# Kernel tuning notes

Hardware: AMD Instinct MI355X
Metric: run time of the kernel (lower is better)

The kernel has to match this reference:

```python
import jax, jax.numpy as jnp
import numpy as np

B, N, M, D, NH, HD = 2, 1024, 1024, 1536, 16, 96
RD = HD // 3  # per-axis rotary dim = 32
EPS = 1e-6
SCALE = HD ** -0.5


def _rmsnorm(y, w):
    return y * jax.lax.rsqrt(jnp.mean(y * y, axis=-1, keepdims=True) + EPS) * w


def _rope_tables(T, H, W):
    # inv_freqs identical for t/h/w since all three dims are RD
    inv_f = 1.0 / (10000.0 ** (jnp.arange(0, RD, 2, dtype=jnp.float32)[: RD // 2] / RD))
    gt, gh, gw = jnp.meshgrid(
        jnp.arange(T, dtype=jnp.float32),
        jnp.arange(H, dtype=jnp.float32),
        jnp.arange(W, dtype=jnp.float32),
        indexing='ij')
    ft = gt.reshape(-1, 1) * inv_f[None, :]  # [L, RD//2]
    fh = gh.reshape(-1, 1) * inv_f[None, :]
    fw = gw.reshape(-1, 1) * inv_f[None, :]
    return (jnp.cos(ft), jnp.sin(ft), jnp.cos(fh), jnp.sin(fh), jnp.cos(fw), jnp.sin(fw))


def _apply_rope(xq, cos, sin):
    # xq: [B, L, NH, RD]; cos/sin: [L, RD//2]
    c = jnp.concatenate([cos, cos], axis=-1)[None, :, None, :]
    s = jnp.concatenate([sin, sin], axis=-1)[None, :, None, :]
    x1, x2 = jnp.split(xq, 2, axis=-1)
    rot = jnp.concatenate([-x2, x1], axis=-1)
    return xq * c + rot * s


def setup_inputs() -> dict:
    key = jax.random.key(0)
    ks = jax.random.split(key, 10)
    w = lambda k: jax.random.normal(k, (D, D), dtype=jnp.float32) * 0.02
    return {
        'cond': jax.random.normal(ks[0], (B, N, D), dtype=jnp.float32),
        'x': jax.random.normal(ks[1], (B, M, D), dtype=jnp.float32),
        'cond_q_w': w(ks[2]), 'cond_k_w': w(ks[3]), 'cond_v_w': w(ks[4]),
        'cond_qnorm_w': jnp.ones((D,), jnp.float32),
        'cond_knorm_w': jnp.ones((D,), jnp.float32),
        'cond_proj_w': w(ks[5]),
        'x_q_w': w(ks[6]), 'x_k_w': w(ks[7]), 'x_v_w': w(ks[8]),
        'x_qnorm_w': jnp.ones((D,), jnp.float32),
        'x_knorm_w': jnp.ones((D,), jnp.float32),
        'x_proj_w': w(ks[9]),
        'T': 2, 'H': 32, 'W': 32,
    }


def reference(cond, x, cond_q_w, cond_k_w, cond_v_w, cond_qnorm_w, cond_knorm_w,
              cond_proj_w, x_q_w, x_k_w, x_v_w, x_qnorm_w, x_knorm_w, x_proj_w,
              T, H, W):
    # dual-stream QKV + RMSNorm (qkv_bias=False, eval -> no dropout)
    cq = _rmsnorm(cond @ cond_q_w, cond_qnorm_w).reshape(B, N, NH, HD)
    ck = _rmsnorm(cond @ cond_k_w, cond_knorm_w).reshape(B, N, NH, HD)
    cv = (cond @ cond_v_w).reshape(B, N, NH, HD)
    xq = _rmsnorm(x @ x_q_w, x_qnorm_w).reshape(B, M, NH, HD)
    xk = _rmsnorm(x @ x_k_w, x_knorm_w).reshape(B, M, NH, HD)
    xv = (x @ x_v_w).reshape(B, M, NH, HD)

    q = jnp.concatenate([cq, xq], axis=1)  # [B, N+M, NH, HD]
    k = jnp.concatenate([ck, xk], axis=1)
    v = jnp.concatenate([cv, xv], axis=1)

    # 3D RoPE: split head_dim into t/h/w thirds and rotate each with its own freqs
    cos_t, sin_t, cos_h, sin_h, cos_w, sin_w = _rope_tables(T, H, W)
    qt, qh, qw = jnp.split(q, 3, axis=-1)
    kt, kh, kw = jnp.split(k, 3, axis=-1)
    q = jnp.concatenate([_apply_rope(qt, cos_t, sin_t),
                         _apply_rope(qh, cos_h, sin_h),
                         _apply_rope(qw, cos_w, sin_w)], axis=-1)
    k = jnp.concatenate([_apply_rope(kt, cos_t, sin_t),
                         _apply_rope(kh, cos_h, sin_h),
                         _apply_rope(kw, cos_w, sin_w)], axis=-1)

    # joint non-causal SDPA
    scores = jnp.einsum('blhd,bmhd->bhlm', q, k) * SCALE
    attn = jax.nn.softmax(scores, axis=-1)
    out = jnp.einsum('bhlm,bmhd->blhd', attn, v).reshape(B, N + M, D)

    cond_out = out[:, :N] @ cond_proj_w
    x_out = out[:, N:] @ x_proj_w
    return cond_out, x_out
```

## Files before the change

kernel.cpp:

```cpp
#include <hip/hip_runtime.h>
#include <stdint.h>

#define DEV __device__ __forceinline__

using f32x4  = __attribute__((ext_vector_type(4))) float;
using f32x16 = __attribute__((ext_vector_type(16))) float;
using bf16x8 = __attribute__((ext_vector_type(8))) short;

DEV ushort f2bf(float f){
  uint32_t u = __float_as_uint(f);
  u += 0x7FFFu + ((u >> 16) & 1u);
  return (ushort)(u >> 16);
}
DEV float bf2f(ushort h){ return __uint_as_float(((uint32_t)h) << 16); }

DEV void async16(const void* g, void* l){
  __builtin_amdgcn_global_load_lds(
      (const __attribute__((address_space(1))) void*)g,
      (__attribute__((address_space(3))) void*)l, 16, 0, 0);
}

union FU { uint4 u; bf16x8 v; };
DEV bf16x8 as_bf16x8(uint a, uint b, uint c, uint d){ FU f; f.u = make_uint4(a,b,c,d); return f.v; }

__global__ __launch_bounds__(256) void k_conv_in(const float* __restrict__ src, ushort* __restrict__ dst){
  int i = (blockIdx.x * 256 + threadIdx.x) * 8;
  float4 a = *(const float4*)(src + i);
  float4 b = *(const float4*)(src + i + 4);
  union { ushort s[8]; uint4 q; } o;
  o.s[0]=f2bf(a.x); o.s[1]=f2bf(a.y); o.s[2]=f2bf(a.z); o.s[3]=f2bf(a.w);
  o.s[4]=f2bf(b.x); o.s[5]=f2bf(b.y); o.s[6]=f2bf(b.z); o.s[7]=f2bf(b.w);
  *(uint4*)(dst + i) = o.q;
}

__global__ __launch_bounds__(256) void k_transpose_w(
    const float* w0, const float* w1, const float* w2, const float* w3,
    const float* w4, const float* w5, const float* w6, const float* w7,
    ushort* __restrict__ dst){
  __shared__ float tile[32][33];
  int z = blockIdx.z;
  const float* src = (z==0)?w0:(z==1)?w1:(z==2)?w2:(z==3)?w3:(z==4)?w4:(z==5)?w5:(z==6)?w6:w7;
  int n0 = blockIdx.x * 32;
  int k0 = blockIdx.y * 32;
  int tx = threadIdx.x;
  int ty = threadIdx.y;
  for (int j = 0; j < 4; ++j)
    tile[ty + j*8][tx] = src[(size_t)(k0 + ty + j*8) * 1536 + n0 + tx];
  __syncthreads();
  ushort* d = dst + (size_t)z * 1536 * 1536;
  for (int j = 0; j < 4; ++j){
    int n = n0 + ty + j*8;
    int k = k0 + tx;
    d[(size_t)n * 1536 + k] = f2bf(tile[tx][ty + j*8]);
  }
}

__global__ __launch_bounds__(512, 2) void k_gemm_qkv(const ushort* __restrict__ inb,
                                                     const ushort* __restrict__ Wt,
                                                     ushort* __restrict__ Y){
  __shared__ ushort As[2][16384];
  __shared__ ushort Bs[2][18432];
  int f = blockIdx.x;
  int nid = (f & 7) * 32 + (f >> 3);
  int z = nid >> 7; int r = nid & 127;
  int my = (r >> 2) & 7, nx = (r >> 5) * 4 + (r & 3);
  const ushort* A = inb + (size_t)z * 2048 * 1536 + (size_t)(my * 256) * 1536;
  const ushort* B = Wt  + (size_t)z * 4608 * 1536 + (size_t)(nx * 288) * 1536;
  ushort* Yt = Y + (size_t)z * 2048 * 4608 + (size_t)(my * 256) * 4608 + nx * 288;
  int tid = threadIdx.x;
  int w = tid >> 6, lane = tid & 63;
  int g = lane >> 4, fr = lane & 15;
  int wm = (w >> 1) * 64, wn = (w & 1) * 144;

  f32x4 acc[4][9] = {};

  auto stageA = [&](int b, int kt){
#pragma unroll
    for (int s = 0; s < 4; ++s){
      int c = s * 512 + tid;
      int row = c >> 3, ch = c & 7;
      async16(A + (size_t)row * 1536 + kt + ((ch ^ (row & 7)) * 8), &As[b][(s*512 + w*64) * 8]);
    }
  };
  auto stageB = [&](int b, int kt){
#pragma unroll
    for (int s = 0; s < 4; ++s){
      int c = s * 512 + tid;
      int row = c >> 3, ch = c & 7;
      async16(B + (size_t)row * 1536 + kt + ((ch ^ (row & 7)) * 8), &Bs[b][(s*512 + w*64) * 8]);
    }
    if (tid < 256){
      int c = 2048 + tid;
      int row = c >> 3, ch = c & 7;
      async16(B + (size_t)row * 1536 + kt + ((ch ^ (row & 7)) * 8), &Bs[b][(2048 + w*64) * 8]);
    }
  };

  stageA(0, 0); stageB(0, 0);
  asm volatile("s_waitcnt vmcnt(0)" ::: "memory");
  __builtin_amdgcn_s_barrier();
  asm volatile("" ::: "memory");

  for (int t = 0; t < 24; ++t){
    int cur = t & 1; int kt1 = (t + 1) * 64;
#pragma unroll
    for (int ks = 0; ks < 2; ++ks){
      bf16x8 af[4], bf[9];
#pragma unroll
      for (int j = 0; j < 4; ++j){
        int row = wm + j*16 + fr;
        af[j] = *(const bf16x8*)&As[cur][(row*8 + ((ks*4 + g) ^ (row & 7))) * 8];
      }
#pragma unroll
      for (int ni = 0; ni < 9; ++ni){
        int row = wn + ni*16 + fr;
        bf[ni] = *(const bf16x8*)&Bs[cur][(row*8 + ((ks*4 + g) ^ (row & 7))) * 8];
      }
      if (t < 23){
        if (ks == 0) stageA(cur ^ 1, kt1);
        else stageB(cur ^ 1, kt1);
      }
      asm volatile("" ::: "memory");
      __builtin_amdgcn_s_barrier();
      asm volatile("" ::: "memory");
      __builtin_amdgcn_s_setprio(1);
#pragma unroll
      for (int ni = 0; ni < 9; ++ni){
#pragma unroll
        for (int j = 0; j < 4; ++j)
          acc[j][ni] = __builtin_amdgcn_mfma_f32_16x16x32_bf16(af[j], bf[ni], acc[j][ni], 0, 0, 0);
      }
      __builtin_amdgcn_s_setprio(0);
      if (ks == 1) asm volatile("s_waitcnt vmcnt(0)" ::: "memory");
      asm volatile("" ::: "memory");
      __builtin_amdgcn_s_barrier();
      asm volatile("" ::: "memory");
    }
  }

#pragma unroll
  for (int mi = 0; mi < 4; ++mi)
#pragma unroll
    for (int ni = 0; ni < 9; ++ni)
#pragma unroll
      for (int rr = 0; rr < 4; ++rr)
        Yt[(size_t)(wm + mi*16 + g*4 + rr) * 4608 + wn + ni*16 + fr] = f2bf(acc[mi][ni][rr]);
}

template<bool OUT_BF16>
DEV void gemm_tile(const ushort* __restrict__ A, const ushort* __restrict__ Bt, void* __restrict__ Cp,
                   int K, int lda, int ldb, int ldc, int m0, int n0){
  __shared__ ushort As[8192];
  __shared__ ushort Bs[8192];
  int tid = threadIdx.x;
  int w = tid >> 6, lane = tid & 63;
  int g = lane >> 4, fr = lane & 15;
  int wm = (w >> 1) * 64, wn = (w & 1) * 64;
  f32x4 acc[4][4] = {};
  for (int kt = 0; kt < K; kt += 64){
    __syncthreads();
#pragma unroll
    for (int i = 0; i < 4; ++i){
      int ci = i * 256 + tid;
      int row = ci >> 3, ch = ci & 7;
      int src8 = (ch ^ (row & 7)) * 8;
      async16(A  + (size_t)(m0 + row) * lda + kt + src8, As + (i*256 + w*64) * 8);
      async16(Bt + (size_t)(n0 + row) * ldb + kt + src8, Bs + (i*256 + w*64) * 8);
    }
    __syncthreads();
#pragma unroll
    for (int ks = 0; ks < 2; ++ks){
      bf16x8 af[4], bf[4];
      int cidx = ((ks*4 + g) ^ (fr & 7)) * 8;
#pragma unroll
      for (int mi = 0; mi < 4; ++mi) af[mi] = *(const bf16x8*)(As + (wm + mi*16 + fr) * 64 + cidx);
#pragma unroll
      for (int ni = 0; ni < 4; ++ni) bf[ni] = *(const bf16x8*)(Bs + (wn + ni*16 + fr) * 64 + cidx);
#pragma unroll
      for (int mi = 0; mi < 4; ++mi)
#pragma unroll
        for (int ni = 0; ni < 4; ++ni)
          acc[mi][ni] = __builtin_amdgcn_mfma_f32_16x16x32_bf16(af[mi], bf[ni], acc[mi][ni], 0, 0, 0);
    }
  }
  int cr = (lane >> 4) * 4, cc2 = lane & 15;
#pragma unroll
  for (int mi = 0; mi < 4; ++mi)
#pragma unroll
    for (int ni = 0; ni < 4; ++ni)
#pragma unroll
      for (int r = 0; r < 4; ++r){
        size_t idx = (size_t)(m0 + wm + mi*16 + cr + r) * ldc + (n0 + wn + ni*16 + cc2);
        if (OUT_BF16) ((ushort*)Cp)[idx] = f2bf(acc[mi][ni][r]);
        else          ((float*)Cp)[idx]  = acc[mi][ni][r];
      }
}

__global__ __launch_bounds__(256) void k_gemm_proj(const ushort* __restrict__ AO, const ushort* __restrict__ Wtp,
                                                   float* __restrict__ out){
  int f = blockIdx.x;
  int nid = (f & 7) * 48 + (f >> 3);
  int z = nid / 96; int rr = nid - z * 96;
  int by = rr / 12; int bx = rr - by * 12;
  int s = z >> 1, bb = z & 1;
  gemm_tile<false>(AO + (size_t)(bb*2048 + s*1024) * 1536, Wtp + (size_t)s * 1536 * 1536,
                   (void*)(out + (size_t)(s*2048 + bb*1024) * 1536), 1536, 1536, 1536, 1536,
                   by * 128, bx * 128);
}

__global__ __launch_bounds__(256) void k_norm_rope(
    const ushort* __restrict__ Y,
    const float* __restrict__ qn_c, const float* __restrict__ kn_c,
    const float* __restrict__ qn_x, const float* __restrict__ kn_x,
    ushort* __restrict__ Qb, ushort* __restrict__ Kb, ushort* __restrict__ Vb){
  int r = blockIdx.x;
  int z = blockIdx.y;
  const ushort* y = Y + ((size_t)z * 2048 + r) * 4608;
  const float* qw = z ? qn_x : qn_c;
  const float* kw = z ? kn_x : kn_c;
  int b = r >> 10;
  int l = (z << 10) + (r & 1023);
  int tid = threadIdx.x;
  __shared__ float cs[48], sn[48];
  if (tid < 48){
    int axis = tid >> 4, fj = tid & 15;
    int pos = (axis == 0) ? (l >> 10) : ((axis == 1) ? ((l >> 5) & 31) : (l & 31));
    float inv = __expf(-(float)fj * 0.5756462732485114f);
    float a = (float)pos * inv;
    sn[tid] = sinf(a); cs[tid] = cosf(a);
  }
  float yq1[3], yq2[3], yk1[3], yk2[3];
  float ssq = 0.f, ssk = 0.f;
#pragma unroll
  for (int i = 0; i < 3; ++i){
    int p = tid + i*256;
    int head = p / 48, rem = p % 48;
    int c1 = head*96 + (rem >> 4)*32 + (rem & 15);
    float a1 = bf2f(y[c1]),        a2 = bf2f(y[c1 + 16]);
    float b1 = bf2f(y[1536 + c1]), b2 = bf2f(y[1536 + c1 + 16]);
    yq1[i]=a1; yq2[i]=a2; yk1[i]=b1; yk2[i]=b2;
    ssq += a1*a1 + a2*a2;
    ssk += b1*b1 + b2*b2;
  }
#pragma unroll
  for (int mm = 1; mm < 64; mm <<= 1){
    ssq += __shfl_xor(ssq, mm);
    ssk += __shfl_xor(ssk, mm);
  }
  __shared__ float red[8];
  int w = tid >> 6;
  if ((tid & 63) == 0){ red[w] = ssq; red[4 + w] = ssk; }
  __syncthreads();
  float scq = rsqrtf((red[0]+red[1]+red[2]+red[3]) * (1.f/1536.f) + 1e-6f);
  float sck = rsqrtf((red[4]+red[5]+red[6]+red[7]) * (1.f/1536.f) + 1e-6f);
  float scqS = scq * 0.1020620726159658f;
#pragma unroll
  for (int i = 0; i < 3; ++i){
    int p = tid + i*256;
    int head = p / 48, rem = p % 48;
    int axis = rem >> 4, fj = rem & 15;
    int c1 = head*96 + axis*32 + fj;
    float c = cs[rem], s = sn[rem];
    size_t rowb = ((size_t)(b*16 + head) * 2048 + l) * 96;
    float a1 = yq1[i] * scqS * qw[c1], a2 = yq2[i] * scqS * qw[c1 + 16];
    Qb[rowb + axis*32 + fj]      = f2bf(a1*c - a2*s);
    Qb[rowb + axis*32 + fj + 16] = f2bf(a2*c + a1*s);
    float b1 = yk1[i] * sck * kw[c1], b2 = yk2[i] * sck * kw[c1 + 16];
    int d1 = axis*32 + fj;
    Kb[rowb + d1]      = f2bf(b1*c - b2*s);
    Kb[rowb + d1 + 16] = f2bf(b2*c + b1*s);
  }
#pragma unroll
  for (int i = 0; i < 6; ++i){
    int cidx = tid + i*256;
    int head = cidx / 96, hd = cidx - head*96;
    Vb[((size_t)(b*16 + head) * 2048 + l) * 96 + hd] = y[3072 + cidx];
  }
}

__global__ __launch_bounds__(256) void k_transpose_v(const ushort* __restrict__ V, ushort* __restrict__ Vt){
  __shared__ ushort t[32][33];
  int bh = blockIdx.z;
  const ushort* src = V + (size_t)bh * 2048 * 96;
  ushort* dst = Vt + (size_t)bh * 96 * 2048;
  int c0 = blockIdx.x * 32;
  int r0 = blockIdx.y * 32;
  int tx = threadIdx.x, ty = threadIdx.y;
  for (int j = 0; j < 4; ++j)
    t[ty + j*8][tx] = src[(size_t)(r0 + ty + j*8) * 96 + c0 + tx];
  __syncthreads();
  for (int j = 0; j < 4; ++j){
    int d = c0 + ty + j*8;
    int l = r0 + tx;
    dst[(size_t)d * 2048 + l] = t[tx][ty + j*8];
  }
}

__global__ __launch_bounds__(256, 2) void k_attn(const ushort* __restrict__ Qb, const ushort* __restrict__ Kb,
                                                 const ushort* __restrict__ Vt, ushort* __restrict__ AO){
  __shared__ ushort Ks[2][6400];
  __shared__ ushort Vs[2][6528];
  int id = blockIdx.x;
  int nid = (id & 7) * 64 + (id >> 3);
  int qt = nid & 15, bh = nid >> 4;
  int b = bh >> 4, head = bh & 15;
  const ushort* Qh = Qb + (size_t)bh * 2048 * 96;
  const ushort* Kh = Kb + (size_t)bh * 2048 * 96;
  const ushort* Vh = Vt + (size_t)bh * 96 * 2048;
  int tid = threadIdx.x;
  int w = tid >> 6, lane = tid & 63;
  int h = lane >> 5, c = lane & 31;
  int q0 = qt * 128 + w * 32;

  bf16x8 qf[6];
#pragma unroll
  for (int kb = 0; kb < 6; ++kb)
    qf[kb] = *(const bf16x8*)(Qh + (size_t)(q0 + c) * 96 + kb*16 + h*8);

  int gko[3], lko[3], gvo[3], lvo[3];
#pragma unroll
  for (int i = 0; i < 3; ++i){
    int fc = i*256 + tid;
    int krow = (fc * 683) >> 13;
    int kc8  = (fc - krow*12) * 8;
    gko[i] = krow*96 + kc8;
    lko[i] = krow*100 + kc8;
    int vrow = fc >> 3;
    int vc8  = (fc & 7) * 8;
    gvo[i] = vrow*2048 + vc8;
    lvo[i] = vrow*68 + (vc8 ^ ((vrow & 7) << 3));
  }
  uint4 kst[3], vst[3];

  auto LOADG = [&](int tt){
#pragma unroll
    for (int i = 0; i < 3; ++i){
      kst[i] = *(const uint4*)(Kh + (size_t)tt*6144 + gko[i]);
      vst[i] = *(const uint4*)(Vh + (size_t)tt*64 + gvo[i]);
    }
  };
  auto WRITE = [&](int buf){
#pragma unroll
    for (int i = 0; i < 3; ++i){
      *(uint2*)(&Ks[buf][lko[i]])     = make_uint2(kst[i].x, kst[i].y);
      *(uint2*)(&Ks[buf][lko[i] + 4]) = make_uint2(kst[i].z, kst[i].w);
      *(uint2*)(&Vs[buf][lvo[i]])     = make_uint2(vst[i].x, vst[i].y);
      *(uint2*)(&Vs[buf][lvo[i] + 4]) = make_uint2(vst[i].z, vst[i].w);
    }
  };
  auto QK = [&](f32x16* sa, int buf){
#pragma unroll
    for (int ni = 0; ni < 2; ++ni){
      f32x16 a = {};
#pragma unroll
      for (int kb = 0; kb < 6; ++kb){
        const ushort* kp = &Ks[buf][(ni*32 + c)*100 + kb*16 + h*8];
        uint2 lo = *(const uint2*)kp;
        uint2 hi = *(const uint2*)(kp + 4);
        a = __builtin_amdgcn_mfma_f32_32x32x16_bf16(as_bf16x8(lo.x, lo.y, hi.x, hi.y), qf[kb], a, 0, 0, 0);
      }
      sa[ni] = a;
    }
  };

  f32x16 o[3] = {};
  float dpart = 0.f;
  f32x16 sa[2];

  LOADG(0);
  WRITE(0);
  LOADG(1);
  asm volatile("s_waitcnt lgkmcnt(0)" ::: "memory");
  __builtin_amdgcn_s_barrier();
  asm volatile("" ::: "memory");
  QK(sa, 0);

  for (int t = 0; t < 32; ++t){
    int cur = t & 1, nxt = cur ^ 1;
    if (t < 31) WRITE(nxt);
    if (t < 30) LOADG(t + 2);
    asm volatile("s_waitcnt lgkmcnt(0)" ::: "memory");
    __builtin_amdgcn_s_barrier();
    asm volatile("" ::: "memory");

    bf16x8 pf[2][2];
#pragma unroll
    for (int ni = 0; ni < 2; ++ni){
      float p[16];
#pragma unroll
      for (int e = 0; e < 16; ++e){
        float x = fmaf(sa[ni][e], 1.44269504f, -14.4269504f);
        asm("v_exp_f32 %0, %1" : "=v"(p[e]) : "v"(x));
      }
      dpart += (((p[0]+p[1])+(p[2]+p[3])) + ((p[4]+p[5])+(p[6]+p[7])))
             + (((p[8]+p[9])+(p[10]+p[11])) + ((p[12]+p[13])+(p[14]+p[15])));
      uint u[8];
#pragma unroll
      for (int e = 0; e < 8; ++e)
        asm("v_cvt_pk_bf16_f32 %0, %1, %2" : "=v"(u[e]) : "v"(p[2*e]), "v"(p[2*e+1]));
      asm("v_permlane32_swap_b32 %0, %1" : "+v"(u[0]), "+v"(u[2]));
      asm("v_permlane32_swap_b32 %0, %1" : "+v"(u[1]), "+v"(u[3]));
      asm("v_permlane32_swap_b32 %0, %1" : "+v"(u[4]), "+v"(u[6]));
      asm("v_permlane32_swap_b32 %0, %1" : "+v"(u[5]), "+v"(u[7]));
      pf[ni][0] = as_bf16x8(u[0], u[1], u[2], u[3]);
      pf[ni][1] = as_bf16x8(u[4], u[5], u[6], u[7]);
    }

    if (t < 31){
      f32x16 na[2];
      QK(na, nxt);
#pragma unroll
      for (int dt = 0; dt < 3; ++dt)
#pragma unroll
        for (int ni = 0; ni < 2; ++ni)
#pragma unroll
          for (int ks = 0; ks < 2; ++ks){
            int chunk = 4*ni + 2*ks + h;
            const ushort* vp = &Vs[cur][(dt*32 + c)*68 + ((chunk ^ (c & 7)) << 3)];
            uint2 lo = *(const uint2*)vp;
            uint2 hi = *(const uint2*)(vp + 4);
            o[dt] = __builtin_amdgcn_mfma_f32_32x32x16_bf16(pf[ni][ks],
                      as_bf16x8(lo.x, lo.y, hi.x, hi.y), o[dt], 0, 0, 0);
          }
      sa[0] = na[0]; sa[1] = na[1];
    } else {
#pragma unroll
      for (int dt = 0; dt < 3; ++dt)
#pragma unroll
        for (int ni = 0; ni < 2; ++ni)
#pragma unroll
          for (int ks = 0; ks < 2; ++ks){
            int chunk = 4*ni + 2*ks + h;
            const ushort* vp = &Vs[cur][(dt*32 + c)*68 + ((chunk ^ (c & 7)) << 3)];
            uint2 lo = *(const uint2*)vp;
            uint2 hi = *(const uint2*)(vp + 4);
            o[dt] = __builtin_amdgcn_mfma_f32_32x32x16_bf16(pf[ni][ks],
                      as_bf16x8(lo.x, lo.y, hi.x, hi.y), o[dt], 0, 0, 0);
          }
    }
    asm volatile("" ::: "memory");
    __builtin_amdgcn_s_barrier();
    asm volatile("" ::: "memory");
  }

  float dtot = dpart + __shfl_xor(dpart, 32);
#pragma unroll
  for (int r = 0; r < 16; ++r){
    int qloc = (r & 3) + 8*(r >> 2) + 4*h;
    float den = __shfl(dtot, qloc);
    float dinv = __builtin_amdgcn_rcpf(den);
    size_t rowoff = ((size_t)b * 2048 + q0 + qloc) * 1536 + head * 96;
#pragma unroll
    for (int dt = 0; dt < 3; ++dt){
      float val = o[dt][r] * dinv;
      uint pk; asm("v_cvt_pk_bf16_f32 %0, %1, %2" : "=v"(pk) : "v"(val), "v"(val));
      AO[rowoff + dt*32 + c] = (ushort)pk;
    }
  }
}

extern "C" void kernel_launch(void* const* d_in, const int* in_sizes, int n_in,
                              void* d_out, int out_size, void* d_ws, size_t ws_size,
                              hipStream_t stream){
  const float* cond = (const float*)d_in[0];
  const float* x    = (const float*)d_in[1];
  const float* wq_c = (const float*)d_in[2];
  const float* wk_c = (const float*)d_in[3];
  const float* wv_c = (const float*)d_in[4];
  const float* qn_c = (const float*)d_in[5];
  const float* kn_c = (const float*)d_in[6];
  const float* wp_c = (const float*)d_in[7];
  const float* wq_x = (const float*)d_in[8];
  const float* wk_x = (const float*)d_in[9];
  const float* wv_x = (const float*)d_in[10];
  const float* qn_x = (const float*)d_in[11];
  const float* kn_x = (const float*)d_in[12];
  const float* wp_x = (const float*)d_in[13];

  char* ws = (char*)d_ws;
  ushort* inb = (ushort*)(ws);
  ushort* Wt  = (ushort*)(ws + 12582912ll);
  ushort* Y   = (ushort*)(ws + 50331648ll);
  ushort* Vt  = (ushort*)(ws + 50331648ll);
  ushort* Qb  = (ushort*)(ws + 88080384ll);
  ushort* Kb  = (ushort*)(ws + 100663296ll);
  ushort* Vb  = (ushort*)(ws + 113246208ll);
  ushort* AO  = inb;

  k_conv_in<<<1536, 256, 0, stream>>>(cond, inb);
  k_conv_in<<<1536, 256, 0, stream>>>(x, inb + 3145728);
  k_transpose_w<<<dim3(48,48,8), dim3(32,8), 0, stream>>>(wq_c, wk_c, wv_c, wq_x, wk_x, wv_x, wp_c, wp_x, Wt);
  k_gemm_qkv<<<256, 512, 0, stream>>>(inb, Wt, Y);
  k_norm_rope<<<dim3(2048,2), 256, 0, stream>>>(Y, qn_c, kn_c, qn_x, kn_x, Qb, Kb, Vb);
  k_transpose_v<<<dim3(3,64,32), dim3(32,8), 0, stream>>>(Vb, Vt);
  k_attn<<<512, 256, 0, stream>>>(Qb, Kb, Vt, AO);
  k_gemm_proj<<<384, 256, 0, stream>>>(AO, Wt + (size_t)9216*1536, (float*)d_out);
  (void)in_sizes; (void)n_in; (void)out_size; (void)ws_size;
}
```

Measured before the change: 207.6 us.

## Transpose V straight from QKV output and widen attention LDS accesses to 128-bit

Measured after the change: 259.3 us. 1.25x slower.

```diff
diff --git a/kernel.cpp b/kernel.cpp
--- a/kernel.cpp
+++ b/kernel.cpp
@@ -212,7 +212,7 @@
     const ushort* __restrict__ Y,
     const float* __restrict__ qn_c, const float* __restrict__ kn_c,
     const float* __restrict__ qn_x, const float* __restrict__ kn_x,
-    ushort* __restrict__ Qb, ushort* __restrict__ Kb, ushort* __restrict__ Vb){
+    ushort* __restrict__ Qb, ushort* __restrict__ Kb){
   int r = blockIdx.x;
   int z = blockIdx.y;
   const ushort* y = Y + ((size_t)z * 2048 + r) * 4608;
@@ -270,36 +270,29 @@
     Kb[rowb + d1]      = f2bf(b1*c - b2*s);
     Kb[rowb + d1 + 16] = f2bf(b2*c + b1*s);
   }
-#pragma unroll
-  for (int i = 0; i < 6; ++i){
-    int cidx = tid + i*256;
-    int head = cidx / 96, hd = cidx - head*96;
-    Vb[((size_t)(b*16 + head) * 2048 + l) * 96 + hd] = y[3072 + cidx];
-  }
-}
-
-__global__ __launch_bounds__(256) void k_transpose_v(const ushort* __restrict__ V, ushort* __restrict__ Vt){
+}
+
+__global__ __launch_bounds__(256) void k_transpose_v(const ushort* __restrict__ Y, ushort* __restrict__ Vt){
   __shared__ ushort t[32][33];
   int bh = blockIdx.z;
-  const ushort* src = V + (size_t)bh * 2048 * 96;
+  int b = bh >> 4, head = bh & 15;
+  int c0 = blockIdx.x * 32;
+  int l0 = blockIdx.y * 32;
+  int z = l0 >> 10;
+  const ushort* src = Y + ((size_t)(z*2048 + b*1024 + (l0 & 1023))) * 4608 + 3072 + head*96 + c0;
   ushort* dst = Vt + (size_t)bh * 96 * 2048;
-  int c0 = blockIdx.x * 32;
-  int r0 = blockIdx.y * 32;
   int tx = threadIdx.x, ty = threadIdx.y;
   for (int j = 0; j < 4; ++j)
-    t[ty + j*8][tx] = src[(size_t)(r0 + ty + j*8) * 96 + c0 + tx];
+    t[ty + j*8][tx] = src[(size_t)(ty + j*8) * 4608 + tx];
   __syncthreads();
-  for (int j = 0; j < 4; ++j){
-    int d = c0 + ty + j*8;
-    int l = r0 + tx;
-    dst[(size_t)d * 2048 + l] = t[tx][ty + j*8];
-  }
+  for (int j = 0; j < 4; ++j)
+    dst[(size_t)(c0 + ty + j*8) * 2048 + l0 + tx] = t[tx][ty + j*8];
 }
 
 __global__ __launch_bounds__(256, 2) void k_attn(const ushort* __restrict__ Qb, const ushort* __restrict__ Kb,
                                                  const ushort* __restrict__ Vt, ushort* __restrict__ AO){
-  __shared__ ushort Ks[2][6400];
-  __shared__ ushort Vs[2][6528];
+  __shared__ ushort Ks[2][64*104];
+  __shared__ ushort Vs[2][96*72];
   int id = blockIdx.x;
   int nid = (id & 7) * 64 + (id >> 3);
   int qt = nid & 15, bh = nid >> 4;
@@ -324,11 +317,11 @@
     int krow = (fc * 683) >> 13;
     int kc8  = (fc - krow*12) * 8;
     gko[i] = krow*96 + kc8;
-    lko[i] = krow*100 + kc8;
+    lko[i] = krow*104 + kc8;
     int vrow = fc >> 3;
     int vc8  = (fc & 7) * 8;
     gvo[i] = vrow*2048 + vc8;
-    lvo[i] = vrow*68 + (vc8 ^ ((vrow & 7) << 3));
+    lvo[i] = vrow*72 + (vc8 ^ ((vrow & 7) << 3));
   }
   uint4 kst[3], vst[3];
 
@@ -342,10 +335,8 @@
   auto WRITE = [&](int buf){
 #pragma unroll
     for (int i = 0; i < 3; ++i){
-      *(uint2*)(&Ks[buf][lko[i]])     = make_uint2(kst[i].x, kst[i].y);
-      *(uint2*)(&Ks[buf][lko[i] + 4]) = make_uint2(kst[i].z, kst[i].w);
-      *(uint2*)(&Vs[buf][lvo[i]])     = make_uint2(vst[i].x, vst[i].y);
-      *(uint2*)(&Vs[buf][lvo[i] + 4]) = make_uint2(vst[i].z, vst[i].w);
+      *(uint4*)(&Ks[buf][lko[i]]) = kst[i];
+      *(uint4*)(&Vs[buf][lvo[i]]) = vst[i];
     }
   };
   auto QK = [&](f32x16* sa, int buf){
@@ -354,10 +345,8 @@
       f32x16 a = {};
 #pragma unroll
       for (int kb = 0; kb < 6; ++kb){
-        const ushort* kp = &Ks[buf][(ni*32 + c)*100 + kb*16 + h*8];
-        uint2 lo = *(const uint2*)kp;
-        uint2 hi = *(const uint2*)(kp + 4);
-        a = __builtin_amdgcn_mfma_f32_32x32x16_bf16(as_bf16x8(lo.x, lo.y, hi.x, hi.y), qf[kb], a, 0, 0, 0);
+        uint4 kq = *(const uint4*)(&Ks[buf][(ni*32 + c)*104 + kb*16 + h*8]);
+        a = __builtin_amdgcn_mfma_f32_32x32x16_bf16(as_bf16x8(kq.x, kq.y, kq.z, kq.w), qf[kb], a, 0, 0, 0);
       }
       sa[ni] = a;
     }
@@ -410,32 +399,28 @@
       f32x16 na[2];
       QK(na, nxt);
 #pragma unroll
-      for (int dt = 0; dt < 3; ++dt)
-#pragma unroll
-        for (int ni = 0; ni < 2; ++ni)
-#pragma unroll
-          for (int ks = 0; ks < 2; ++ks){
+      for (int ni = 0; ni < 2; ++ni)
+#pragma unroll
+        for (int ks = 0; ks < 2; ++ks)
+#pragma unroll
+          for (int dt = 0; dt < 3; ++dt){
             int chunk = 4*ni + 2*ks + h;
-            const ushort* vp = &Vs[cur][(dt*32 + c)*68 + ((chunk ^ (c & 7)) << 3)];
-            uint2 lo = *(const uint2*)vp;
-            uint2 hi = *(const uint2*)(vp + 4);
+            uint4 vq = *(const uint4*)(&Vs[cur][(dt*32 + c)*72 + ((chunk ^ (c & 7)) << 3)]);
             o[dt] = __builtin_amdgcn_mfma_f32_32x32x16_bf16(pf[ni][ks],
-                      as_bf16x8(lo.x, lo.y, hi.x, hi.y), o[dt], 0, 0, 0);
+                      as_bf16x8(vq.x, vq.y, vq.z, vq.w), o[dt], 0, 0, 0);
           }
       sa[0] = na[0]; sa[1] = na[1];
     } else {
 #pragma unroll
-      for (int dt = 0; dt < 3; ++dt)
-#pragma unroll
-        for (int ni = 0; ni < 2; ++ni)
-#pragma unroll
-          for (int ks = 0; ks < 2; ++ks){
+      for (int ni = 0; ni < 2; ++ni)
+#pragma unroll
+        for (int ks = 0; ks < 2; ++ks)
+#pragma unroll
+          for (int dt = 0; dt < 3; ++dt){
             int chunk = 4*ni + 2*ks + h;
-            const ushort* vp = &Vs[cur][(dt*32 + c)*68 + ((chunk ^ (c & 7)) << 3)];
-            uint2 lo = *(const uint2*)vp;
-            uint2 hi = *(const uint2*)(vp + 4);
+            uint4 vq = *(const uint4*)(&Vs[cur][(dt*32 + c)*72 + ((chunk ^ (c & 7)) << 3)]);
             o[dt] = __builtin_amdgcn_mfma_f32_32x32x16_bf16(pf[ni][ks],
-                      as_bf16x8(lo.x, lo.y, hi.x, hi.y), o[dt], 0, 0, 0);
+                      as_bf16x8(vq.x, vq.y, vq.z, vq.w), o[dt], 0, 0, 0);
           }
     }
     asm volatile("" ::: "memory");
@@ -481,18 +466,17 @@
   ushort* inb = (ushort*)(ws);
   ushort* Wt  = (ushort*)(ws + 12582912ll);
   ushort* Y   = (ushort*)(ws + 50331648ll);
-  ushort* Vt  = (ushort*)(ws + 50331648ll);
   ushort* Qb  = (ushort*)(ws + 88080384ll);
   ushort* Kb  = (ushort*)(ws + 100663296ll);
-  ushort* Vb  = (ushort*)(ws + 113246208ll);
+  ushort* Vt  = (ushort*)(ws + 113246208ll);
   ushort* AO  = inb;
 
   k_conv_in<<<1536, 256, 0, stream>>>(cond, inb);
   k_conv_in<<<1536, 256, 0, stream>>>(x, inb + 3145728);
   k_transpose_w<<<dim3(48,48,8), dim3(32,8), 0, stream>>>(wq_c, wk_c, wv_c, wq_x, wk_x, wv_x, wp_c, wp_x, Wt);
   k_gemm_qkv<<<256, 512, 0, stream>>>(inb, Wt, Y);
-  k_norm_rope<<<dim3(2048,2), 256, 0, stream>>>(Y, qn_c, kn_c, qn_x, kn_x, Qb, Kb, Vb);
-  k_transpose_v<<<dim3(3,64,32), dim3(32,8), 0, stream>>>(Vb, Vt);
+  k_norm_rope<<<dim3(2048,2), 256, 0, stream>>>(Y, qn_c, kn_c, qn_x, kn_x, Qb, Kb);
+  k_transpose_v<<<dim3(3,64,32), dim3(32,8), 0, stream>>>(Y, Vt);
   k_attn<<<512, 256, 0, stream>>>(Qb, Kb, Vt, AO);
   k_gemm_proj<<<384, 256, 0, stream>>>(AO, Wt + (size_t)9216*1536, (float*)d_out);
   (void)in_sizes; (void)n_in; (void)out_size; (void)ws_size;
```
